# Kernel optimization log

Measured on AMD Instinct MI355X. Metric: run time of the kernel, lower is better.

The kernel has to match this reference:

```python
import jax, jax.numpy as jnp
import numpy as np
import itertools

B, N, IN_DIM, H_DIM, OUT_DIM, K = 64, 32, 128, 512, 256, 2


def _uniform(key, shape, fan_in):
    bound = 1.0 / np.sqrt(fan_in)
    return jax.random.uniform(key, shape, jnp.float32, -bound, bound)


def setup_inputs() -> dict:
    key = jax.random.key(0)
    ks = jax.random.split(key, 7)
    x = jax.random.normal(ks[0], (B, N, IN_DIM), jnp.float32)
    W1 = _uniform(ks[1], (IN_DIM * K, H_DIM), IN_DIM * K)
    b1 = _uniform(ks[2], (H_DIM,), IN_DIM * K)
    W2 = _uniform(ks[3], (H_DIM, H_DIM), H_DIM)
    b2 = _uniform(ks[4], (H_DIM,), H_DIM)
    W3 = _uniform(ks[5], (H_DIM, OUT_DIM), H_DIM)
    b3 = _uniform(ks[6], (OUT_DIM,), H_DIM)
    return {"x": x, "W1": W1, "b1": b1, "W2": W2, "b2": b2, "W3": W3, "b3": b3}


def reference(x, W1, b1, W2, b2, W3, b3):
    n = x.shape[1]
    # all k-permutations of set indices, itertools order: [P, K], P = N*(N-1) for K=2
    perm = jnp.asarray(np.array(list(itertools.permutations(range(n), K)), dtype=np.int32))
    # gather: [B, P, K, in_dim] -> flatten last two dims -> [B, P, K*in_dim]
    xp = x[:, perm, :].reshape(x.shape[0], perm.shape[0], K * x.shape[2])
    h = jax.nn.relu(jnp.einsum('bpf,fh->bph', xp, W1) + b1)
    h = jax.nn.relu(jnp.einsum('bph,hg->bpg', h, W2) + b2)
    out = jnp.einsum('bpg,go->bpo', h, W3) + b3
    return out.sum(axis=1)  # sum over permutations -> [B, out_dim]
```

## Files before the change

### kernel.cpp

```cpp
#include <hip/hip_runtime.h>

#define BB 64
#define NN 32
#define IND 128
#define HD 512
#define OD 256
#define NPERM 992

typedef __attribute__((ext_vector_type(8))) _Float16 half8;
typedef __attribute__((ext_vector_type(4))) _Float16 half4;
typedef __attribute__((ext_vector_type(16))) float f32x16;

typedef __attribute__((address_space(3))) char lds_char_t;
typedef __attribute__((address_space(1))) const char gbl_char_t;

__device__ __forceinline__ void glds16(const void* g, void* l) {
    __builtin_amdgcn_global_load_lds((gbl_char_t*)g, (lds_char_t*)l, 16, 0, 0);
}

#define WAITVM8 asm volatile("s_waitcnt vmcnt(8)" ::: "memory")
#define WAITVM4 asm volatile("s_waitcnt vmcnt(4)" ::: "memory")
#define WAITVM1 asm volatile("s_waitcnt vmcnt(1)" ::: "memory")
#define WAITLGKM asm volatile("s_waitcnt lgkmcnt(0)" ::: "memory")
#define RBAR __builtin_amdgcn_s_barrier()

__device__ __forceinline__ half8 relu8(half8 x) {
    half8 z = 0;
    return __builtin_elementwise_max(x, z);
}

#define XTO 69632
__global__ __launch_bounds__(512, 4) void kprep(
    const float* __restrict__ x, const float* __restrict__ W1, const float* __restrict__ b1,
    const float* __restrict__ W2, _Float16* __restrict__ W2t,
    const float* __restrict__ b3, float* __restrict__ out,
    _Float16* __restrict__ U, _Float16* __restrict__ Vo) {
    __shared__ char smem[(256 + 32) * 272];
    const int bid = blockIdx.x;
    const int t = threadIdx.x;

    if (bid >= 256) {
        const int bid2 = bid - 256;
        float (*tile)[65] = (float (*)[65])smem;
        if (t < 256) out[(size_t)bid2 * OD + t] = (float)NPERM * b3[t];
        const int k0 = (bid2 & 7) * 64, c0 = (bid2 >> 3) * 64;
        const int cin = t & 63, r0 = (t >> 6) * 8;
#pragma unroll
        for (int rr = 0; rr < 8; ++rr)
            tile[r0 + rr][cin] = W2[(size_t)(k0 + r0 + rr) * HD + c0 + cin];
        __syncthreads();
        const int kout = t & 63;
#pragma unroll
        for (int rr = 0; rr < 8; ++rr) {
            int c = r0 + rr;
            W2t[(size_t)(c0 + c) * HD + k0 + kout] = (_Float16)tile[kout][c];
        }
        return;
    }

    const int g = bid & 3, b = bid >> 2;
    const int h0 = (g & 1) * 256;
    const int koff = (g >> 1) * 128;

    {
        const int n = t >> 4, c8 = (t & 15) * 8;
        const float* src = x + ((size_t)(b * NN + n)) * IND + c8;
        float4 f0 = *(const float4*)src;
        float4 f1 = *(const float4*)(src + 4);
        half8 h;
        h[0] = (_Float16)f0.x; h[1] = (_Float16)f0.y;
        h[2] = (_Float16)f0.z; h[3] = (_Float16)f0.w;
        h[4] = (_Float16)f1.x; h[5] = (_Float16)f1.y;
        h[6] = (_Float16)f1.z; h[7] = (_Float16)f1.w;
        *(half8*)(smem + XTO + n * 272 + c8 * 2) = h;
    }
    {
        const int ht = t & 63, ktb = t >> 6;
#pragma unroll
        for (int it = 0; it < 4; ++it) {
            const int kt = ktb + it * 8;
            const float* wsrc = W1 + (size_t)(koff + kt * 4) * HD + h0 + ht * 4;
            float4 v0 = *(const float4*)(wsrc);
            float4 v1 = *(const float4*)(wsrc + HD);
            float4 v2 = *(const float4*)(wsrc + 2 * HD);
            float4 v3 = *(const float4*)(wsrc + 3 * HD);
            char* wdst = smem + (size_t)(ht * 4) * 272 + kt * 8;
            half4 o0 = {(_Float16)v0.x, (_Float16)v1.x, (_Float16)v2.x, (_Float16)v3.x};
            half4 o1 = {(_Float16)v0.y, (_Float16)v1.y, (_Float16)v2.y, (_Float16)v3.y};
            half4 o2 = {(_Float16)v0.z, (_Float16)v1.z, (_Float16)v2.z, (_Float16)v3.z};
            half4 o3 = {(_Float16)v0.w, (_Float16)v1.w, (_Float16)v2.w, (_Float16)v3.w};
            *(half4*)(wdst) = o0;
            *(half4*)(wdst + 272) = o1;
            *(half4*)(wdst + 544) = o2;
            *(half4*)(wdst + 816) = o3;
        }
    }
    __syncthreads();

    const int lane = t & 63, wv = t >> 6;
    const int l31 = lane & 31, hi = lane >> 5;
    const char* abase = smem + XTO + (size_t)l31 * 272 + hi * 16;
    const char* bbase = smem + (size_t)(wv * 32 + l31) * 272 + hi * 16;

    f32x16 acc;
#pragma unroll
    for (int r = 0; r < 16; ++r) acc[r] = 0.f;
#pragma unroll
    for (int ks = 0; ks < 8; ++ks) {
        half8 a  = *(const half8*)(abase + ks * 32);
        half8 bf = *(const half8*)(bbase + ks * 32);
        acc = __builtin_amdgcn_mfma_f32_32x32x16_f16(a, bf, acc, 0, 0, 0);
    }
    const int hglob = h0 + wv * 32 + l31;
    const float bias = (g < 2) ? b1[hglob] : 0.f;
    _Float16* dst = ((g < 2) ? U : Vo) + (size_t)b * NN * HD + hglob;
#pragma unroll
    for (int r = 0; r < 16; ++r) {
        int row = (r & 3) + 8 * (r >> 2) + 4 * hi;
        dst[(size_t)row * HD] = (_Float16)(acc[r] + bias);
    }
}

#define SLOT0 65536
#define SLOT1 98304
__global__ __launch_bounds__(512, 2) void k2(
    const _Float16* __restrict__ Ug, const _Float16* __restrict__ Vg,
    const _Float16* __restrict__ W2t, const float* __restrict__ b2,
    const float* __restrict__ W3, float* __restrict__ out) {
    __shared__ char smb[131072];
    __shared__ float red[8][64];
    __shared__ float hred[64];

    const int bp = blockIdx.x;
    const int cb0 = blockIdx.y * 64;
    const int t = threadIdx.x;
    const int lane = t & 63, wid = t >> 6;
    const int l31 = lane & 31, hi = lane >> 5;
    const int lh = lane >> 5, lm = lane & 31;
    const unsigned sw = (unsigned)((l31 & 15) << 4);

    auto issueB = [&](int kh) {
#pragma unroll
        for (int ii = 0; ii < 4; ++ii) {
            int r = wid * 8 + ii * 2 + lh;
            const char* src = (const char*)W2t + (size_t)(cb0 + r) * 1024 + kh * 512
                              + ((lm * 16) ^ ((r & 15) << 4));
            glds16(src, smb + kh * 32768 + (wid * 8 + ii * 2) * 512);
        }
    };
    auto issueUV = [&](int bb, int kh, unsigned slotOff) {
#pragma unroll
        for (int ii = 0; ii < 2; ++ii) {
            int r = wid * 4 + ii * 2 + lh;
            const char* src = (const char*)Vg + (size_t)(bb * NN + r) * 1024 + kh * 512
                              + ((lm * 16) ^ ((r & 15) << 4));
            glds16(src, smb + slotOff + (wid * 4 + ii * 2) * 512);
        }
#pragma unroll
        for (int ii = 0; ii < 2; ++ii) {
            int r = wid * 4 + ii * 2 + lh;
            const char* src = (const char*)Ug + (size_t)(bb * NN + r) * 1024 + kh * 512 + lm * 16;
            glds16(src, smb + slotOff + 16384 + (wid * 4 + ii * 2) * 512);
        }
    };

    const int bA = bp * 2, bB = bp * 2 + 1;
    issueB(0);
    issueUV(bA, 0, SLOT0);
    issueB(1);
    issueUV(bA, 1, SLOT1);
    WAITVM8;
    RBAR;

    f32x16 acc[4][2];
    auto resetAcc = [&]() {
#pragma unroll
        for (int rf = 0; rf < 4; ++rf)
#pragma unroll
            for (int cf = 0; cf < 2; ++cf)
#pragma unroll
                for (int r = 0; r < 16; ++r) acc[rf][cf][r] = 0.f;
    };

    auto compute = [&](unsigned slotOff, int kh) {
        const unsigned ub = slotOff + 16384u + (unsigned)(wid * 4 * 512) + (unsigned)(hi * 16);
        const unsigned vb = slotOff + (unsigned)(l31 * 512);
        const unsigned bb0 = (unsigned)(kh * 32768 + l31 * 512);
        const unsigned bb1 = (unsigned)(kh * 32768 + (32 + l31) * 512);

        half8 pU0, pU1, pU2, pU3, pV, pB0, pB1;
        {
            unsigned kx = ((unsigned)(hi * 16)) ^ sw;
            pU0 = *(const half8*)(smb + ub + 0 * 512);
            pU1 = *(const half8*)(smb + ub + 1 * 512);
            pU2 = *(const half8*)(smb + ub + 2 * 512);
            pU3 = *(const half8*)(smb + ub + 3 * 512);
            pV  = *(const half8*)(smb + vb + kx);
            pB0 = *(const half8*)(smb + bb0 + kx);
            pB1 = *(const half8*)(smb + bb1 + kx);
        }
#pragma unroll
        for (int kk = 0; kk < 16; ++kk) {
            half8 cU0 = pU0, cU1 = pU1, cU2 = pU2, cU3 = pU3;
            half8 cV = pV, cB0 = pB0, cB1 = pB1;
            if (kk < 15) {
                int kn = kk + 1;
                unsigned kx = ((unsigned)(kn * 32 + hi * 16)) ^ sw;
                pU0 = *(const half8*)(smb + ub + 0 * 512 + kn * 32);
                pU1 = *(const half8*)(smb + ub + 1 * 512 + kn * 32);
                pU2 = *(const half8*)(smb + ub + 2 * 512 + kn * 32);
                pU3 = *(const half8*)(smb + ub + 3 * 512 + kn * 32);
                pV  = *(const half8*)(smb + vb + kx);
                pB0 = *(const half8*)(smb + bb0 + kx);
                pB1 = *(const half8*)(smb + bb1 + kx);
            }

            __builtin_amdgcn_s_setprio(1);
            half8 af0 = relu8(cU0 + cV);
            acc[0][0] = __builtin_amdgcn_mfma_f32_32x32x16_f16(af0, cB0, acc[0][0], 0, 0, 0);
            acc[0][1] = __builtin_amdgcn_mfma_f32_32x32x16_f16(af0, cB1, acc[0][1], 0, 0, 0);
            half8 af1 = relu8(cU1 + cV);
            acc[1][0] = __builtin_amdgcn_mfma_f32_32x32x16_f16(af1, cB0, acc[1][0], 0, 0, 0);
            acc[1][1] = __builtin_amdgcn_mfma_f32_32x32x16_f16(af1, cB1, acc[1][1], 0, 0, 0);
            half8 af2 = relu8(cU2 + cV);
            acc[2][0] = __builtin_amdgcn_mfma_f32_32x32x16_f16(af2, cB0, acc[2][0], 0, 0, 0);
            acc[2][1] = __builtin_amdgcn_mfma_f32_32x32x16_f16(af2, cB1, acc[2][1], 0, 0, 0);
            half8 af3 = relu8(cU3 + cV);
            acc[3][0] = __builtin_amdgcn_mfma_f32_32x32x16_f16(af3, cB0, acc[3][0], 0, 0, 0);
            acc[3][1] = __builtin_amdgcn_mfma_f32_32x32x16_f16(af3, cB1, acc[3][1], 0, 0, 0);
            __builtin_amdgcn_s_setprio(0);

#pragma unroll
            for (int gq = 0; gq < 4; ++gq) {
                __builtin_amdgcn_sched_group_barrier(0x002, 8, 0);
                __builtin_amdgcn_sched_group_barrier(0x008, 2, 0);
            }
        }
    };

    auto sums_gemv = [&]() -> float {
        float scf[2];
#pragma unroll
        for (int cf = 0; cf < 2; ++cf) {
            int col = cb0 + cf * 32 + l31;
            float b2v = b2[col];
            float s = 0.f;
#pragma unroll
            for (int rf = 0; rf < 4; ++rf) {
                int i_idx = wid * 4 + rf;
#pragma unroll
                for (int r = 0; r < 16; ++r) {
                    int row = (r & 3) + 8 * (r >> 2) + 4 * hi;
                    float h2 = fmaxf(acc[rf][cf][r] + b2v, 0.f);
                    if (row != i_idx) s += h2;
                }
            }
            s += __shfl_xor(s, 32);
            scf[cf] = s;
        }
        if (lane < 32) {
            red[wid][l31] = scf[0];
            red[wid][32 + l31] = scf[1];
        }
        WAITLGKM; RBAR;
        if (t < 64) {
            float hsum = 0.f;
#pragma unroll
            for (int w = 0; w < 8; ++w) hsum += red[w][t];
            hred[t] = hsum;
        }
        WAITLGKM; RBAR;
        int o = t & 255, gg = t >> 8;
        const float* w3p = W3 + ((size_t)(cb0 + gg * 32)) * OD + o;
        float a = 0.f;
#pragma unroll 8
        for (int j = 0; j < 32; ++j)
            a += hred[gg * 32 + j] * w3p[(size_t)j * OD];
        return a;
    };

    resetAcc();
    compute(SLOT0, 0);
    RBAR;
    issueUV(bB, 0, SLOT0);
    WAITVM4;
    RBAR;
    compute(SLOT1, 1);
    RBAR;
    issueUV(bB, 1, SLOT1);
    float a0 = sums_gemv();
    WAITVM4;
    atomicAdd(&out[(size_t)bA * OD + (t & 255)], a0);
    RBAR;
    resetAcc();
    compute(SLOT0, 0);
    WAITVM1;
    RBAR;
    compute(SLOT1, 1);
    float a1 = sums_gemv();
    atomicAdd(&out[(size_t)bB * OD + (t & 255)], a1);
}

extern "C" void kernel_launch(void* const* d_in, const int* in_sizes, int n_in,
                              void* d_out, int out_size, void* d_ws, size_t ws_size,
                              hipStream_t stream) {
    const float* x  = (const float*)d_in[0];
    const float* W1 = (const float*)d_in[1];
    const float* b1 = (const float*)d_in[2];
    const float* W2 = (const float*)d_in[3];
    const float* b2 = (const float*)d_in[4];
    const float* W3 = (const float*)d_in[5];
    const float* b3 = (const float*)d_in[6];
    float* out = (float*)d_out;

    _Float16* U   = (_Float16*)d_ws;
    _Float16* V   = U + (size_t)BB * NN * HD;
    _Float16* W2t = V + (size_t)BB * NN * HD;

    hipLaunchKernelGGL(kprep, dim3(320), dim3(512), 0, stream,
                       x, W1, b1, W2, W2t, b3, out, U, V);
    hipLaunchKernelGGL(k2, dim3(32, 8), dim3(512), 0, stream, U, V, W2t, b2, W3, out);
}
```

Before: 42.04 us.

## Split k2 by i-half into 256-thread blocks, read U/V from global directly

```diff
diff --git a/kernel.cpp b/kernel.cpp
--- a/kernel.cpp
+++ b/kernel.cpp
@@ -19,8 +19,7 @@
 }
 
 #define WAITVM8 asm volatile("s_waitcnt vmcnt(8)" ::: "memory")
-#define WAITVM4 asm volatile("s_waitcnt vmcnt(4)" ::: "memory")
-#define WAITVM1 asm volatile("s_waitcnt vmcnt(1)" ::: "memory")
+#define WAITVM0 asm volatile("s_waitcnt vmcnt(0)" ::: "memory")
 #define WAITLGKM asm volatile("s_waitcnt lgkmcnt(0)" ::: "memory")
 #define RBAR __builtin_amdgcn_s_barrier()
 
@@ -121,54 +120,32 @@
     }
 }
 
-#define SLOT0 65536
-#define SLOT1 98304
-__global__ __launch_bounds__(512, 2) void k2(
+__global__ __launch_bounds__(256, 2) void k2(
     const _Float16* __restrict__ Ug, const _Float16* __restrict__ Vg,
     const _Float16* __restrict__ W2t, const float* __restrict__ b2,
     const float* __restrict__ W3, float* __restrict__ out) {
-    __shared__ char smb[131072];
-    __shared__ float red[8][64];
+    __shared__ char smb[65536];
+    __shared__ float red[4][64];
     __shared__ float hred[64];
 
     const int bp = blockIdx.x;
     const int cb0 = blockIdx.y * 64;
+    const int ih = blockIdx.z;
     const int t = threadIdx.x;
     const int lane = t & 63, wid = t >> 6;
     const int l31 = lane & 31, hi = lane >> 5;
     const int lh = lane >> 5, lm = lane & 31;
     const unsigned sw = (unsigned)((l31 & 15) << 4);
 
-    auto issueB = [&](int kh) {
-#pragma unroll
-        for (int ii = 0; ii < 4; ++ii) {
-            int r = wid * 8 + ii * 2 + lh;
+#pragma unroll
+    for (int kh = 0; kh < 2; ++kh)
+#pragma unroll
+        for (int ii = 0; ii < 8; ++ii) {
+            int r = wid * 16 + ii * 2 + lh;
             const char* src = (const char*)W2t + (size_t)(cb0 + r) * 1024 + kh * 512
                               + ((lm * 16) ^ ((r & 15) << 4));
-            glds16(src, smb + kh * 32768 + (wid * 8 + ii * 2) * 512);
-        }
-    };
-    auto issueUV = [&](int bb, int kh, unsigned slotOff) {
-#pragma unroll
-        for (int ii = 0; ii < 2; ++ii) {
-            int r = wid * 4 + ii * 2 + lh;
-            const char* src = (const char*)Vg + (size_t)(bb * NN + r) * 1024 + kh * 512
-                              + ((lm * 16) ^ ((r & 15) << 4));
-            glds16(src, smb + slotOff + (wid * 4 + ii * 2) * 512);
-        }
-#pragma unroll
-        for (int ii = 0; ii < 2; ++ii) {
-            int r = wid * 4 + ii * 2 + lh;
-            const char* src = (const char*)Ug + (size_t)(bb * NN + r) * 1024 + kh * 512 + lm * 16;
-            glds16(src, smb + slotOff + 16384 + (wid * 4 + ii * 2) * 512);
-        }
-    };
-
-    const int bA = bp * 2, bB = bp * 2 + 1;
-    issueB(0);
-    issueUV(bA, 0, SLOT0);
-    issueB(1);
-    issueUV(bA, 1, SLOT1);
+            glds16(src, smb + kh * 32768 + (wid * 16 + ii * 2) * 512);
+        }
     WAITVM8;
     RBAR;
 
@@ -182,20 +159,22 @@
                 for (int r = 0; r < 16; ++r) acc[rf][cf][r] = 0.f;
     };
 
-    auto compute = [&](unsigned slotOff, int kh) {
-        const unsigned ub = slotOff + 16384u + (unsigned)(wid * 4 * 512) + (unsigned)(hi * 16);
-        const unsigned vb = slotOff + (unsigned)(l31 * 512);
+    auto compute = [&](int bb, int kh) {
+        const char* u0 = (const char*)(Ug + (size_t)(bb * NN + ih * 16 + wid * 4) * HD
+                                       + kh * 256) + hi * 16;
+        const char* vbase = (const char*)(Vg + (size_t)(bb * NN + l31) * HD + kh * 256)
+                            + hi * 16;
         const unsigned bb0 = (unsigned)(kh * 32768 + l31 * 512);
         const unsigned bb1 = (unsigned)(kh * 32768 + (32 + l31) * 512);
 
         half8 pU0, pU1, pU2, pU3, pV, pB0, pB1;
         {
             unsigned kx = ((unsigned)(hi * 16)) ^ sw;
-            pU0 = *(const half8*)(smb + ub + 0 * 512);
-            pU1 = *(const half8*)(smb + ub + 1 * 512);
-            pU2 = *(const half8*)(smb + ub + 2 * 512);
-            pU3 = *(const half8*)(smb + ub + 3 * 512);
-            pV  = *(const half8*)(smb + vb + kx);
+            pU0 = *(const half8*)(u0 + 0 * 1024);
+            pU1 = *(const half8*)(u0 + 1 * 1024);
+            pU2 = *(const half8*)(u0 + 2 * 1024);
+            pU3 = *(const half8*)(u0 + 3 * 1024);
+            pV  = *(const half8*)(vbase);
             pB0 = *(const half8*)(smb + bb0 + kx);
             pB1 = *(const half8*)(smb + bb1 + kx);
         }
@@ -206,11 +185,11 @@
             if (kk < 15) {
                 int kn = kk + 1;
                 unsigned kx = ((unsigned)(kn * 32 + hi * 16)) ^ sw;
-                pU0 = *(const half8*)(smb + ub + 0 * 512 + kn * 32);
-                pU1 = *(const half8*)(smb + ub + 1 * 512 + kn * 32);
-                pU2 = *(const half8*)(smb + ub + 2 * 512 + kn * 32);
-                pU3 = *(const half8*)(smb + ub + 3 * 512 + kn * 32);
-                pV  = *(const half8*)(smb + vb + kx);
+                pU0 = *(const half8*)(u0 + 0 * 1024 + kn * 32);
+                pU1 = *(const half8*)(u0 + 1 * 1024 + kn * 32);
+                pU2 = *(const half8*)(u0 + 2 * 1024 + kn * 32);
+                pU3 = *(const half8*)(u0 + 3 * 1024 + kn * 32);
+                pV  = *(const half8*)(vbase + kn * 32);
                 pB0 = *(const half8*)(smb + bb0 + kx);
                 pB1 = *(const half8*)(smb + bb1 + kx);
             }
@@ -247,7 +226,7 @@
             float s = 0.f;
 #pragma unroll
             for (int rf = 0; rf < 4; ++rf) {
-                int i_idx = wid * 4 + rf;
+                int i_idx = ih * 16 + wid * 4 + rf;
 #pragma unroll
                 for (int r = 0; r < 16; ++r) {
                     int row = (r & 3) + 8 * (r >> 2) + 4 * hi;
@@ -266,39 +245,32 @@
         if (t < 64) {
             float hsum = 0.f;
 #pragma unroll
-            for (int w = 0; w < 8; ++w) hsum += red[w][t];
+            for (int w = 0; w < 4; ++w) hsum += red[w][t];
             hred[t] = hsum;
         }
         WAITLGKM; RBAR;
-        int o = t & 255, gg = t >> 8;
-        const float* w3p = W3 + ((size_t)(cb0 + gg * 32)) * OD + o;
         float a = 0.f;
+        const float* w3p = W3 + (size_t)cb0 * OD + t;
 #pragma unroll 8
-        for (int j = 0; j < 32; ++j)
-            a += hred[gg * 32 + j] * w3p[(size_t)j * OD];
+        for (int j = 0; j < 64; ++j)
+            a += hred[j] * w3p[(size_t)j * OD];
         return a;
     };
 
+    const int bA = bp * 2, bB = bp * 2 + 1;
+
     resetAcc();
-    compute(SLOT0, 0);
+    compute(bA, 0);
+    WAITVM0;
     RBAR;
-    issueUV(bB, 0, SLOT0);
-    WAITVM4;
-    RBAR;
-    compute(SLOT1, 1);
-    RBAR;
-    issueUV(bB, 1, SLOT1);
+    compute(bA, 1);
     float a0 = sums_gemv();
-    WAITVM4;
-    atomicAdd(&out[(size_t)bA * OD + (t & 255)], a0);
-    RBAR;
+    atomicAdd(&out[(size_t)bA * OD + t], a0);
     resetAcc();
-    compute(SLOT0, 0);
-    WAITVM1;
-    RBAR;
-    compute(SLOT1, 1);
+    compute(bB, 0);
+    compute(bB, 1);
     float a1 = sums_gemv();
-    atomicAdd(&out[(size_t)bB * OD + (t & 255)], a1);
+    atomicAdd(&out[(size_t)bB * OD + t], a1);
 }
 
 extern "C" void kernel_launch(void* const* d_in, const int* in_sizes, int n_in,
@@ -319,5 +291,5 @@
 
     hipLaunchKernelGGL(kprep, dim3(320), dim3(512), 0, stream,
                        x, W1, b1, W2, W2t, b3, out, U, V);
-    hipLaunchKernelGGL(k2, dim3(32, 8), dim3(512), 0, stream, U, V, W2t, b2, W3, out);
-}
+    hipLaunchKernelGGL(k2, dim3(32, 8, 2), dim3(256), 0, stream, U, V, W2t, b2, W3, out);
+}
```

Measured after the change: 48.55 us. 15.5% more time.

## Fuse prep and main kernels into one cooperative kernel with grid sync

Applied to the files above, without the earlier changes.

```diff
diff --git a/kernel.cpp b/kernel.cpp
--- a/kernel.cpp
+++ b/kernel.cpp
@@ -1,4 +1,7 @@
 #include <hip/hip_runtime.h>
+#include <hip/hip_cooperative_groups.h>
+
+namespace cg = cooperative_groups;
 
 #define BB 64
 #define NN 32
@@ -20,6 +23,7 @@
 
 #define WAITVM8 asm volatile("s_waitcnt vmcnt(8)" ::: "memory")
 #define WAITVM4 asm volatile("s_waitcnt vmcnt(4)" ::: "memory")
+#define WAITVM2 asm volatile("s_waitcnt vmcnt(2)" ::: "memory")
 #define WAITVM1 asm volatile("s_waitcnt vmcnt(1)" ::: "memory")
 #define WAITLGKM asm volatile("s_waitcnt lgkmcnt(0)" ::: "memory")
 #define RBAR __builtin_amdgcn_s_barrier()
@@ -30,114 +34,107 @@
 }
 
 #define XTO 69632
-__global__ __launch_bounds__(512, 4) void kprep(
-    const float* __restrict__ x, const float* __restrict__ W1, const float* __restrict__ b1,
-    const float* __restrict__ W2, _Float16* __restrict__ W2t,
-    const float* __restrict__ b3, float* __restrict__ out,
-    _Float16* __restrict__ U, _Float16* __restrict__ Vo) {
-    __shared__ char smem[(256 + 32) * 272];
-    const int bid = blockIdx.x;
-    const int t = threadIdx.x;
-
-    if (bid >= 256) {
-        const int bid2 = bid - 256;
-        float (*tile)[65] = (float (*)[65])smem;
-        if (t < 256) out[(size_t)bid2 * OD + t] = (float)NPERM * b3[t];
-        const int k0 = (bid2 & 7) * 64, c0 = (bid2 >> 3) * 64;
-        const int cin = t & 63, r0 = (t >> 6) * 8;
-#pragma unroll
-        for (int rr = 0; rr < 8; ++rr)
-            tile[r0 + rr][cin] = W2[(size_t)(k0 + r0 + rr) * HD + c0 + cin];
-        __syncthreads();
-        const int kout = t & 63;
-#pragma unroll
-        for (int rr = 0; rr < 8; ++rr) {
-            int c = r0 + rr;
-            W2t[(size_t)(c0 + c) * HD + k0 + kout] = (_Float16)tile[kout][c];
-        }
-        return;
-    }
-
-    const int g = bid & 3, b = bid >> 2;
-    const int h0 = (g & 1) * 256;
-    const int koff = (g >> 1) * 128;
-
-    {
-        const int n = t >> 4, c8 = (t & 15) * 8;
-        const float* src = x + ((size_t)(b * NN + n)) * IND + c8;
-        float4 f0 = *(const float4*)src;
-        float4 f1 = *(const float4*)(src + 4);
-        half8 h;
-        h[0] = (_Float16)f0.x; h[1] = (_Float16)f0.y;
-        h[2] = (_Float16)f0.z; h[3] = (_Float16)f0.w;
-        h[4] = (_Float16)f1.x; h[5] = (_Float16)f1.y;
-        h[6] = (_Float16)f1.z; h[7] = (_Float16)f1.w;
-        *(half8*)(smem + XTO + n * 272 + c8 * 2) = h;
-    }
-    {
-        const int ht = t & 63, ktb = t >> 6;
-#pragma unroll
-        for (int it = 0; it < 4; ++it) {
-            const int kt = ktb + it * 8;
-            const float* wsrc = W1 + (size_t)(koff + kt * 4) * HD + h0 + ht * 4;
-            float4 v0 = *(const float4*)(wsrc);
-            float4 v1 = *(const float4*)(wsrc + HD);
-            float4 v2 = *(const float4*)(wsrc + 2 * HD);
-            float4 v3 = *(const float4*)(wsrc + 3 * HD);
-            char* wdst = smem + (size_t)(ht * 4) * 272 + kt * 8;
-            half4 o0 = {(_Float16)v0.x, (_Float16)v1.x, (_Float16)v2.x, (_Float16)v3.x};
-            half4 o1 = {(_Float16)v0.y, (_Float16)v1.y, (_Float16)v2.y, (_Float16)v3.y};
-            half4 o2 = {(_Float16)v0.z, (_Float16)v1.z, (_Float16)v2.z, (_Float16)v3.z};
-            half4 o3 = {(_Float16)v0.w, (_Float16)v1.w, (_Float16)v2.w, (_Float16)v3.w};
-            *(half4*)(wdst) = o0;
-            *(half4*)(wdst + 272) = o1;
-            *(half4*)(wdst + 544) = o2;
-            *(half4*)(wdst + 816) = o3;
-        }
-    }
-    __syncthreads();
-
-    const int lane = t & 63, wv = t >> 6;
-    const int l31 = lane & 31, hi = lane >> 5;
-    const char* abase = smem + XTO + (size_t)l31 * 272 + hi * 16;
-    const char* bbase = smem + (size_t)(wv * 32 + l31) * 272 + hi * 16;
-
-    f32x16 acc;
-#pragma unroll
-    for (int r = 0; r < 16; ++r) acc[r] = 0.f;
-#pragma unroll
-    for (int ks = 0; ks < 8; ++ks) {
-        half8 a  = *(const half8*)(abase + ks * 32);
-        half8 bf = *(const half8*)(bbase + ks * 32);
-        acc = __builtin_amdgcn_mfma_f32_32x32x16_f16(a, bf, acc, 0, 0, 0);
-    }
-    const int hglob = h0 + wv * 32 + l31;
-    const float bias = (g < 2) ? b1[hglob] : 0.f;
-    _Float16* dst = ((g < 2) ? U : Vo) + (size_t)b * NN * HD + hglob;
-#pragma unroll
-    for (int r = 0; r < 16; ++r) {
-        int row = (r & 3) + 8 * (r >> 2) + 4 * hi;
-        dst[(size_t)row * HD] = (_Float16)(acc[r] + bias);
-    }
-}
-
+#define TILEO 78336
 #define SLOT0 65536
 #define SLOT1 98304
-__global__ __launch_bounds__(512, 2) void k2(
-    const _Float16* __restrict__ Ug, const _Float16* __restrict__ Vg,
-    const _Float16* __restrict__ W2t, const float* __restrict__ b2,
-    const float* __restrict__ W3, float* __restrict__ out) {
+__global__ __launch_bounds__(512, 2) void kfused(
+    const float* __restrict__ x, const float* __restrict__ W1, const float* __restrict__ b1,
+    const float* __restrict__ W2, const float* __restrict__ b2,
+    const float* __restrict__ W3, const float* __restrict__ b3,
+    float* __restrict__ out,
+    _Float16* __restrict__ Ug, _Float16* __restrict__ Vg, _Float16* __restrict__ W2t) {
     __shared__ char smb[131072];
     __shared__ float red[8][64];
     __shared__ float hred[64];
 
-    const int bp = blockIdx.x;
-    const int cb0 = blockIdx.y * 64;
+    const int bid = blockIdx.x;
     const int t = threadIdx.x;
     const int lane = t & 63, wid = t >> 6;
     const int l31 = lane & 31, hi = lane >> 5;
     const int lh = lane >> 5, lm = lane & 31;
     const unsigned sw = (unsigned)((l31 & 15) << 4);
+
+    {
+        const int g = bid & 3, b = bid >> 2;
+        const int h0 = (g & 1) * 256;
+        const int koff = (g >> 1) * 128;
+
+        {
+            const int n = t >> 4, c8 = (t & 15) * 8;
+            const float* src = x + ((size_t)(b * NN + n)) * IND + c8;
+            float4 f0 = *(const float4*)src;
+            float4 f1 = *(const float4*)(src + 4);
+            half8 h;
+            h[0] = (_Float16)f0.x; h[1] = (_Float16)f0.y;
+            h[2] = (_Float16)f0.z; h[3] = (_Float16)f0.w;
+            h[4] = (_Float16)f1.x; h[5] = (_Float16)f1.y;
+            h[6] = (_Float16)f1.z; h[7] = (_Float16)f1.w;
+            *(half8*)(smb + XTO + n * 272 + c8 * 2) = h;
+        }
+        {
+            const int ht = t & 63, ktb = t >> 6;
+#pragma unroll
+            for (int it = 0; it < 4; ++it) {
+                const int kt = ktb + it * 8;
+                const float* wsrc = W1 + (size_t)(koff + kt * 4) * HD + h0 + ht * 4;
+                float4 v0 = *(const float4*)(wsrc);
+                float4 v1 = *(const float4*)(wsrc + HD);
+                float4 v2 = *(const float4*)(wsrc + 2 * HD);
+                float4 v3 = *(const float4*)(wsrc + 3 * HD);
+                char* wdst = smb + (size_t)(ht * 4) * 272 + kt * 8;
+                half4 o0 = {(_Float16)v0.x, (_Float16)v1.x, (_Float16)v2.x, (_Float16)v3.x};
+                half4 o1 = {(_Float16)v0.y, (_Float16)v1.y, (_Float16)v2.y, (_Float16)v3.y};
+                half4 o2 = {(_Float16)v0.z, (_Float16)v1.z, (_Float16)v2.z, (_Float16)v3.z};
+                half4 o3 = {(_Float16)v0.w, (_Float16)v1.w, (_Float16)v2.w, (_Float16)v3.w};
+                *(half4*)(wdst) = o0;
+                *(half4*)(wdst + 272) = o1;
+                *(half4*)(wdst + 544) = o2;
+                *(half4*)(wdst + 816) = o3;
+            }
+        }
+        float (*tile)[33] = (float (*)[33])(smb + TILEO);
+        const int tr = bid & 15, tc = bid >> 4;
+        {
+            const int r = t >> 4, c0 = t & 15;
+            tile[r][c0]      = W2[(size_t)(tr * 32 + r) * HD + tc * 32 + c0];
+            tile[r][c0 + 16] = W2[(size_t)(tr * 32 + r) * HD + tc * 32 + c0 + 16];
+        }
+        __syncthreads();
+
+        {
+            const int wv = wid;
+            const char* abase = (const char*)smb + XTO + (size_t)l31 * 272 + hi * 16;
+            const char* bbase = (const char*)smb + (size_t)(wv * 32 + l31) * 272 + hi * 16;
+            f32x16 acc;
+#pragma unroll
+            for (int r = 0; r < 16; ++r) acc[r] = 0.f;
+#pragma unroll
+            for (int ks = 0; ks < 8; ++ks) {
+                half8 a  = *(const half8*)(abase + ks * 32);
+                half8 bf = *(const half8*)(bbase + ks * 32);
+                acc = __builtin_amdgcn_mfma_f32_32x32x16_f16(a, bf, acc, 0, 0, 0);
+            }
+            const int hglob = h0 + wv * 32 + l31;
+            const float bias = (g < 2) ? b1[hglob] : 0.f;
+            _Float16* dst = ((g < 2) ? Ug : Vg) + (size_t)b * NN * HD + hglob;
+#pragma unroll
+            for (int r = 0; r < 16; ++r) {
+                int row = (r & 3) + 8 * (r >> 2) + 4 * hi;
+                dst[(size_t)row * HD] = (_Float16)(acc[r] + bias);
+            }
+        }
+        {
+            const int r = t >> 4, c0 = t & 15;
+            W2t[(size_t)(tc * 32 + r) * HD + tr * 32 + c0]      = (_Float16)tile[c0][r];
+            W2t[(size_t)(tc * 32 + r) * HD + tr * 32 + c0 + 16] = (_Float16)tile[c0 + 16][r];
+        }
+        if (g == 0 && t < 256) out[(size_t)b * OD + t] = (float)NPERM * b3[t];
+    }
+
+    cg::this_grid().sync();
+
+    const int bp = bid & 31;
+    const int cb0 = (bid >> 5) * 64;
 
     auto issueB = [&](int kh) {
 #pragma unroll
@@ -182,7 +179,7 @@
                 for (int r = 0; r < 16; ++r) acc[rf][cf][r] = 0.f;
     };
 
-    auto compute = [&](unsigned slotOff, int kh) {
+    auto compute = [&](int kh, unsigned slotOff) {
         const unsigned ub = slotOff + 16384u + (unsigned)(wid * 4 * 512) + (unsigned)(hi * 16);
         const unsigned vb = slotOff + (unsigned)(l31 * 512);
         const unsigned bb0 = (unsigned)(kh * 32768 + l31 * 512);
@@ -280,12 +277,12 @@
     };
 
     resetAcc();
-    compute(SLOT0, 0);
+    compute(0, SLOT0);
     RBAR;
     issueUV(bB, 0, SLOT0);
     WAITVM4;
     RBAR;
-    compute(SLOT1, 1);
+    compute(1, SLOT1);
     RBAR;
     issueUV(bB, 1, SLOT1);
     float a0 = sums_gemv();
@@ -293,10 +290,10 @@
     atomicAdd(&out[(size_t)bA * OD + (t & 255)], a0);
     RBAR;
     resetAcc();
-    compute(SLOT0, 0);
+    compute(0, SLOT0);
     WAITVM1;
     RBAR;
-    compute(SLOT1, 1);
+    compute(1, SLOT1);
     float a1 = sums_gemv();
     atomicAdd(&out[(size_t)bB * OD + (t & 255)], a1);
 }
@@ -317,7 +314,7 @@
     _Float16* V   = U + (size_t)BB * NN * HD;
     _Float16* W2t = V + (size_t)BB * NN * HD;
 
-    hipLaunchKernelGGL(kprep, dim3(320), dim3(512), 0, stream,
-                       x, W1, b1, W2, W2t, b3, out, U, V);
-    hipLaunchKernelGGL(k2, dim3(32, 8), dim3(512), 0, stream, U, V, W2t, b2, W3, out);
+    void* args[] = {(void*)&x, (void*)&W1, (void*)&b1, (void*)&W2, (void*)&b2,
+                    (void*)&W3, (void*)&b3, (void*)&out, (void*)&U, (void*)&V, (void*)&W2t};
+    hipLaunchCooperativeKernel((const void*)kfused, dim3(256), dim3(512), args, 0, stream);
 }
```

After: 76.58 us. +82.2%, slower.
